# Optimization experiments

Hardware: AMD Instinct MI355X
Metric: run time of the kernel (lower is better)

The kernel has to match this reference:

```python
import jax, jax.numpy as jnp
import numpy as np

N = 100000   # nodes
E = 1600000  # edges (avg degree 16)
F = 64       # input feature dim
H = 64       # hidden dim
O = 64       # conv output dim
C = 2        # channels (x.shape[1])
S = 1000     # number of subgraphs
M = 64       # nodes per subgraph
MH = 128     # MLP hidden
OUT = 1      # MLP output


def setup_inputs() -> dict:
    key = jax.random.key(0)
    ks = jax.random.split(key, 16)
    x = jax.random.normal(ks[0], (N, C, F), jnp.float32)
    edge_index = jax.random.randint(ks[1], (2, E), 0, N, dtype=jnp.int32)
    edge_weight = jax.random.uniform(ks[2], (E,), jnp.float32)
    subG_node = jax.random.randint(ks[3], (S, M), 0, N, dtype=jnp.int32)
    s1 = 1.0 / np.sqrt(F)
    s2 = 1.0 / np.sqrt(H)
    sm1 = 1.0 / np.sqrt(O)
    sm2 = 1.0 / np.sqrt(MH)
    return {
        "x": x,
        "edge_index": edge_index,
        "edge_weight": edge_weight,
        "subG_node": subG_node,
        "W1": jax.random.normal(ks[4], (F, H), jnp.float32) * s1,
        "b1": jnp.zeros((H,), jnp.float32),
        "gn_w": jnp.ones((H,), jnp.float32),
        "gn_b": jnp.zeros((H,), jnp.float32),
        "gn_ms": jnp.ones((H,), jnp.float32),
        "W2": jax.random.normal(ks[5], (H, O), jnp.float32) * s2,
        "b2": jnp.zeros((O,), jnp.float32),
        "mW1": jax.random.normal(ks[6], (O, MH), jnp.float32) * sm1,
        "mb1": jnp.zeros((MH,), jnp.float32),
        "mW2": jax.random.normal(ks[7], (MH, OUT), jnp.float32) * sm2,
        "mb2": jnp.zeros((OUT,), jnp.float32),
    }


def _graph_norm(h, w, b, ms, eps=1e-5):
    # PyG GraphNorm over all nodes (single graph): per-feature stats
    mean = jnp.mean(h, axis=0, keepdims=True)
    out = h - ms * mean
    var = jnp.mean(out * out, axis=0, keepdims=True)
    return w * out * jax.lax.rsqrt(var + eps) + b


def _gcn_layer(h, src, dst, norm, self_norm, W, b, n):
    # GCNConv: h' = D^-1/2 (A + I) D^-1/2 (h @ W) + b
    hw = h @ W                                   # [N, out]
    msg = norm[:, None] * hw[src]                # [E, out] gather
    agg = jax.ops.segment_sum(msg, dst, num_segments=n)  # scatter-add
    agg = agg + self_norm[:, None] * hw          # self-loop term
    return agg + b


def reference(x, edge_index, edge_weight, subG_node,
              W1, b1, gn_w, gn_b, gn_ms, W2, b2, mW1, mb1, mW2, mb2):
    n = x.shape[0]
    src, dst = edge_index[0], edge_index[1]
    # symmetric GCN normalization with self-loops of weight 1
    deg = jax.ops.segment_sum(edge_weight, dst, num_segments=n) + 1.0
    dinv = jax.lax.rsqrt(deg)
    norm = dinv[src] * edge_weight * dinv[dst]   # [E]
    self_norm = dinv * dinv                      # [N]

    def conv_channel(xc):  # xc: [N, F]
        h = _gcn_layer(xc, src, dst, norm, self_norm, W1, b1, n)
        h = _graph_norm(h, gn_w, gn_b, gn_ms)
        h = jax.nn.relu(h)
        return _gcn_layer(h, src, dst, norm, self_norm, W2, b2, n)

    emb = jax.vmap(conv_channel, in_axes=1, out_axes=1)(x)  # [N, C, O]
    emb = jnp.mean(emb, axis=1)                              # [N, O]
    # subgraph pooling: sp @ emb == sum of member-node embeddings
    pooled = jnp.sum(emb[subG_node], axis=1)                 # [S, O]
    h = jax.nn.relu(pooled @ mW1 + mb1)
    return h @ mW2 + mb2                                     # [S, 1]
```

## Files before the change

### kernel.cpp

```cpp
#include <hip/hip_runtime.h>
#include <hip/hip_fp16.h>

#define NNODES 100000
#define NEDGES 1600000
#define NSUB   1000
#define MSUB   64
#define MHID   128

#define WSHIFT 9
#define WIN    512
#define NWIN   ((NNODES + 511) >> 9)
#define NBLK   256
#define CHUNK  (NEDGES / NBLK)

typedef _Float16 f16x8 __attribute__((ext_vector_type(8)));
typedef float    f32x4 __attribute__((ext_vector_type(4)));


__global__ __launch_bounds__(256) void k_hist(const int* __restrict__ dst,
                                              int* __restrict__ block_counts,
                                              int* __restrict__ cursor) {
    __shared__ int hist[NWIN];
    int t = threadIdx.x, b = blockIdx.x;
    if (b == 0 && t == 0) *cursor = 0;
    for (int i = t; i < NWIN; i += 256) hist[i] = 0;
    __syncthreads();
    int e0 = b * CHUNK;
    for (int e = e0 + t; e < e0 + CHUNK; e += 256)
        atomicAdd(&hist[dst[e] >> WSHIFT], 1);
    __syncthreads();
    for (int i = t; i < NWIN; i += 256) block_counts[b * NWIN + i] = hist[i];
}

__global__ __launch_bounds__(256) void k_off(const int* __restrict__ block_counts,
                                             int* __restrict__ cursor,
                                             int* __restrict__ win_base,
                                             int* __restrict__ win_lim,
                                             int* __restrict__ block_off,
                                             float* __restrict__ stats,
                                             unsigned* __restrict__ edges) {
    __shared__ int arr[256];
    __shared__ int red[256];
    __shared__ int base_s;
    int t = threadIdx.x, w = blockIdx.x;
    int own = block_counts[t * NWIN + w];
    arr[t] = own; red[t] = own;
    __syncthreads();
    for (int off = 128; off > 0; off >>= 1) {
        if (t < off) red[t] += red[t + off];
        __syncthreads();
    }
    if (t == 0) base_s = atomicAdd(cursor, red[0]);
    for (int off = 1; off < 256; off <<= 1) {
        int v = (t >= off) ? arr[t - off] : 0;
        __syncthreads();
        arr[t] += v;
        __syncthreads();
    }
    int base = base_s;
    block_off[t * NWIN + w] = base + arr[t] - own;
    if (t == 0) { win_base[w] = base; win_lim[w] = base + red[0]; }
    if (w == 0) {
        stats[t] = 0.0f; stats[t + 256] = 0.0f;
        if (t < 16) edges[NEDGES + t] = 0u;
    }
}

__global__ __launch_bounds__(256) void k_scatter(const int* __restrict__ src,
                                                 const int* __restrict__ dst,
                                                 const float* __restrict__ ew,
                                                 const int* __restrict__ block_off,
                                                 int2* __restrict__ esw) {
    __shared__ int myoff[NWIN];
    int t = threadIdx.x, b = blockIdx.x;
    for (int i = t; i < NWIN; i += 256) myoff[i] = block_off[b * NWIN + i];
    __syncthreads();
    int e0 = b * CHUNK;
    for (int e = e0 + t; e < e0 + CHUNK; e += 256) {
        int d = dst[e];
        int w = d >> WSHIFT;
        int pos = atomicAdd(&myoff[w], 1);
        int dl = d - (w << WSHIFT);
        esw[pos] = make_int2((dl << 17) | src[e], __float_as_int(ew[e]));
    }
}

__global__ __launch_bounds__(256) void k_fill2(const int* __restrict__ win_base,
                                               const int* __restrict__ win_lim,
                                               const int2* __restrict__ esw,
                                               unsigned* __restrict__ edges,
                                               int* __restrict__ row_ptr,
                                               int* __restrict__ cnt,
                                               float* __restrict__ dinv) {
    __shared__ int   cnt_l[WIN];
    __shared__ int   sc[WIN];
    __shared__ int   fill_l[WIN];
    __shared__ float degw[WIN];
    int t = threadIdx.x, w = blockIdx.x;
    #pragma unroll
    for (int i = t; i < WIN; i += 256) { cnt_l[i] = 0; fill_l[i] = 0; degw[i] = 0.f; }
    __syncthreads();
    int e0 = win_base[w], e1 = win_lim[w];
    for (int e = e0 + t; e < e1; e += 256) {
        int2 v = esw[e];
        int dl = ((unsigned)v.x) >> 17;
        atomicAdd(&cnt_l[dl], 1);
        atomicAdd(&degw[dl], __int_as_float(v.y));
    }
    __syncthreads();
    sc[t] = cnt_l[t]; sc[t + 256] = cnt_l[t + 256];
    __syncthreads();
    for (int off = 1; off < WIN; off <<= 1) {
        int v0 = (t >= off) ? sc[t - off] : 0;
        int v1 = (t + 256 >= off) ? sc[t + 256 - off] : 0;
        __syncthreads();
        sc[t] += v0; sc[t + 256] += v1;
        __syncthreads();
    }
    sc[t]       = e0 + sc[t]       - cnt_l[t];
    sc[t + 256] = e0 + sc[t + 256] - cnt_l[t + 256];
    __syncthreads();
    for (int e = e0 + t; e < e1; e += 256) {
        int2 v = esw[e];
        int dl = ((unsigned)v.x) >> 17;
        int pos = sc[dl] + atomicAdd(&fill_l[dl], 1);
        int wq = __float2int_rn(__int_as_float(v.y) * 32767.0f);
        edges[pos] = ((unsigned)wq << 17) | ((unsigned)v.x & 0x1FFFFu);
    }
    __syncthreads();
    #pragma unroll
    for (int i = t; i < WIN; i += 256) {
        int node = (w << WSHIFT) + i;
        if (node < NNODES) {
            row_ptr[node] = sc[i];
            cnt[node]     = cnt_l[i];
            dinv[node]    = rsqrtf(degw[i] + 1.0f);
        }
    }
}


template <bool TR>
__global__ __launch_bounds__(256) void k_gemm(const void* __restrict__ Xv,
                                              const float* __restrict__ Wg,
                                              const float* __restrict__ dinv,
                                              _Float16* __restrict__ Y,
                                              const float* __restrict__ stats,
                                              const float* __restrict__ gn_w,
                                              const float* __restrict__ gn_b,
                                              const float* __restrict__ gn_ms) {
    __shared__ __align__(16) _Float16 ob[4][16 * 72];
    int t = threadIdx.x;
    int wave = t >> 6, lane = t & 63;
    int m = lane & 15, q = lane >> 4;

    f16x8 bf[2][4];
    #pragma unroll
    for (int kb = 0; kb < 2; kb++)
        #pragma unroll
        for (int nt = 0; nt < 4; nt++)
            #pragma unroll
            for (int j = 0; j < 8; j++)
                bf[kb][nt][j] = (_Float16)Wg[(kb * 32 + q * 8 + j) * 64 + nt * 16 + m];

    float ca[16], cb[16];
    if constexpr (TR) {
        int c = m & 1;
        const float inv_n = 1.0f / (float)NNODES;
        #pragma unroll
        for (int kb = 0; kb < 2; kb++)
            #pragma unroll
            for (int j = 0; j < 8; j++) {
                int k = kb * 32 + q * 8 + j;
                int col = c * 64 + k;
                float mean = stats[col] * inv_n;
                float eh2  = stats[128 + col] * inv_n;
                float ms   = gn_ms[k];
                float mm   = ms * mean;
                float var  = eh2 - 2.0f * mm * mean + mm * mm;
                float A = gn_w[k] * rsqrtf(var + 1e-5f);
                ca[kb * 8 + j] = A;
                cb[kb * 8 + j] = gn_b[k] - A * mm;
            }
    }

    int tile = blockIdx.x * 4 + wave;
    int row0 = tile * 16;

    f16x8 af[2];
    if constexpr (!TR) {
        const float* xp = (const float*)Xv + (size_t)(row0 + m) * 64;
        #pragma unroll
        for (int kb = 0; kb < 2; kb++) {
            float4 u0 = *(const float4*)(xp + kb * 32 + q * 8);
            float4 u1 = *(const float4*)(xp + kb * 32 + q * 8 + 4);
            af[kb][0] = (_Float16)u0.x; af[kb][1] = (_Float16)u0.y;
            af[kb][2] = (_Float16)u0.z; af[kb][3] = (_Float16)u0.w;
            af[kb][4] = (_Float16)u1.x; af[kb][5] = (_Float16)u1.y;
            af[kb][6] = (_Float16)u1.z; af[kb][7] = (_Float16)u1.w;
        }
    } else {
        const _Float16* xp = (const _Float16*)Xv + (size_t)(row0 + m) * 64;
        #pragma unroll
        for (int kb = 0; kb < 2; kb++) {
            f16x8 v = *(const f16x8*)(xp + kb * 32 + q * 8);
            #pragma unroll
            for (int j = 0; j < 8; j++) {
                float f = (float)v[j];
                f = fmaxf(ca[kb * 8 + j] * f + cb[kb * 8 + j], 0.0f);
                af[kb][j] = (_Float16)f;
            }
        }
    }

    f32x4 acc[4];
    #pragma unroll
    for (int nt = 0; nt < 4; nt++) {
        acc[nt] = (f32x4){0.f, 0.f, 0.f, 0.f};
        acc[nt] = __builtin_amdgcn_mfma_f32_16x16x32_f16(af[0], bf[0][nt], acc[nt], 0, 0, 0);
        acc[nt] = __builtin_amdgcn_mfma_f32_16x16x32_f16(af[1], bf[1][nt], acc[nt], 0, 0, 0);
    }

    float dv[4];
    #pragma unroll
    for (int i = 0; i < 4; i++) dv[i] = dinv[(row0 + q * 4 + i) >> 1];

    _Float16* obw = ob[wave];
    #pragma unroll
    for (int nt = 0; nt < 4; nt++)
        #pragma unroll
        for (int i = 0; i < 4; i++)
            obw[(q * 4 + i) * 72 + nt * 16 + m] = (_Float16)(acc[nt][i] * dv[i]);
    __syncthreads();

    _Float16* yp = Y + (size_t)row0 * 64;
    #pragma unroll
    for (int s = 0; s < 2; s++) {
        int c8 = s * 64 + lane;
        int r = c8 >> 3, cg = c8 & 7;
        uint4 v = *(const uint4*)(obw + r * 72 + cg * 8);
        *(uint4*)(yp + (size_t)r * 64 + cg * 8) = v;
    }
}


__global__ __launch_bounds__(256) void k_prop(const __half* __restrict__ hw,
                                              const float* __restrict__ bias,
                                              const float* __restrict__ dinv,
                                              const int* __restrict__ row_ptr,
                                              const int* __restrict__ cnt,
                                              const unsigned* __restrict__ edges,
                                              __half* __restrict__ agg) {
    int t = threadIdx.x;
    int lane = t & 63;
    int n = __builtin_amdgcn_readfirstlane(blockIdx.x * 4 + (t >> 6));
    if (n >= NNODES) return;

    int f = lane * 2;
    int feat = f & 63;
    const float qs = 1.0f / 32767.0f;

    float2 bv = *(const float2*)(bias + feat);
    float dv = dinv[n];
    float2 self = __half22float2(*(const __half2*)(hw + (size_t)n * 128 + f));
    float acc0 = self.x;
    float acc1 = self.y;

    int start = row_ptr[n];
    int cn    = cnt[n];
    const unsigned* pp = edges + start;

    int full = cn & ~15;
    int p = 0;
    for (; p < full; p += 16) {
        unsigned e[16];
        #pragma unroll
        for (int i = 0; i < 16; i++) e[i] = pp[p + i];
        float2 h[16];
        #pragma unroll
        for (int i = 0; i < 16; i++) {
            int s = (int)(e[i] & 0x1FFFFu);
            h[i] = __half22float2(*(const __half2*)(hw + (size_t)s * 128 + f));
        }
        #pragma unroll
        for (int i = 0; i < 16; i++) {
            float w = (float)(e[i] >> 17) * qs;
            acc0 += w * h[i].x;
            acc1 += w * h[i].y;
        }
    }
    if (p < cn) {
        unsigned e[16];
        #pragma unroll
        for (int i = 0; i < 16; i++) e[i] = pp[p + i];
        float2 h[16];
        #pragma unroll
        for (int i = 0; i < 16; i++) {
            int s = (int)(e[i] & 0x1FFFFu);
            h[i] = __half22float2(*(const __half2*)(hw + (size_t)s * 128 + f));
        }
        #pragma unroll
        for (int i = 0; i < 16; i++) {
            float w = ((p + i) < cn) ? (float)(e[i] >> 17) * qs : 0.0f;
            acc0 += w * h[i].x;
            acc1 += w * h[i].y;
        }
    }

    *(__half2*)(agg + (size_t)n * 128 + f) =
        __floats2half2_rn(dv * acc0 + bv.x, dv * acc1 + bv.y);
}


__global__ __launch_bounds__(256) void k_stats(const __half* __restrict__ agg,
                                               float* __restrict__ stats) {
    __shared__ float ls[16][128];
    __shared__ float lq[16][128];
    int t = threadIdx.x;
    int cb = (t & 15) * 8;
    int rg = t >> 4;
    float s[8], q[8];
    #pragma unroll
    for (int i = 0; i < 8; i++) { s[i] = 0.f; q[i] = 0.f; }
    for (int r = blockIdx.x * 16 + rg; r < NNODES; r += gridDim.x * 16) {
        uint4 u = *(const uint4*)(agg + (size_t)r * 128 + cb);
        const __half2* h2 = (const __half2*)&u;
        #pragma unroll
        for (int i = 0; i < 4; i++) {
            float2 v = __half22float2(h2[i]);
            s[2*i]   += v.x; q[2*i]   += v.x * v.x;
            s[2*i+1] += v.y; q[2*i+1] += v.y * v.y;
        }
    }
    #pragma unroll
    for (int i = 0; i < 8; i++) { ls[rg][cb + i] = s[i]; lq[rg][cb + i] = q[i]; }
    __syncthreads();
    if (t < 128) {
        float a = 0.f, b = 0.f;
        #pragma unroll
        for (int g = 0; g < 16; g++) { a += ls[g][t]; b += lq[g][t]; }
        atomicAdd(&stats[t], a);
        atomicAdd(&stats[128 + t], b);
    }
}


__global__ __launch_bounds__(256) void k_head(const __half* __restrict__ agg,
                                              const int* __restrict__ subg,
                                              const float* __restrict__ mW1,
                                              const float* __restrict__ mb1,
                                              const float* __restrict__ mW2,
                                              const float* __restrict__ mb2,
                                              float* __restrict__ out) {
    __shared__ int   idx[64];
    __shared__ float pl[4][64];
    __shared__ float red[128];
    int s = blockIdx.x, t = threadIdx.x;
    if (t < 64) idx[t] = subg[s * 64 + t];
    __syncthreads();
    int j = t & 63, grp = t >> 6;
    float acc = 0.f;
    #pragma unroll
    for (int m = grp * 16; m < grp * 16 + 16; m++) {
        int n = idx[m];
        acc += __half2float(agg[(size_t)n * 128 + j]) +
               __half2float(agg[(size_t)n * 128 + 64 + j]);
    }
    pl[grp][j] = acc * 0.5f;
    __syncthreads();
    if (t < 64) pl[0][t] = pl[0][t] + pl[1][t] + pl[2][t] + pl[3][t];
    __syncthreads();
    if (t < 128) {
        float h = mb1[t];
        #pragma unroll
        for (int k = 0; k < 64; k++) h += pl[0][k] * mW1[k * 128 + t];
        h = fmaxf(h, 0.0f);
        red[t] = h * mW2[t];
    }
    __syncthreads();
    for (int off = 64; off > 0; off >>= 1) {
        if (t < off) red[t] += red[t + off];
        __syncthreads();
    }
    if (t == 0) out[s] = red[0] + mb2[0];
}


extern "C" void kernel_launch(void* const* d_in, const int* in_sizes, int n_in,
                              void* d_out, int out_size, void* d_ws, size_t ws_size,
                              hipStream_t stream) {
    const float* x     = (const float*)d_in[0];
    const int*   ei    = (const int*)d_in[1];
    const float* ew    = (const float*)d_in[2];
    const int*   subg  = (const int*)d_in[3];
    const float* W1    = (const float*)d_in[4];
    const float* b1    = (const float*)d_in[5];
    const float* gn_w  = (const float*)d_in[6];
    const float* gn_b  = (const float*)d_in[7];
    const float* gn_ms = (const float*)d_in[8];
    const float* W2    = (const float*)d_in[9];
    const float* b2    = (const float*)d_in[10];
    const float* mW1   = (const float*)d_in[11];
    const float* mb1   = (const float*)d_in[12];
    const float* mW2   = (const float*)d_in[13];
    const float* mb2   = (const float*)d_in[14];
    float* out = (float*)d_out;

    char* w = (char*)d_ws;
    size_t off = 0;
    auto alloc = [&](size_t bytes) {
        void* p = w + off;
        off = (off + bytes + 255) & ~(size_t)255;
        return p;
    };
    float*    dinv    = (float*)   alloc((size_t)NNODES * 4);
    int*      cnt     = (int*)     alloc((size_t)NNODES * 4);
    int*      row_ptr = (int*)     alloc((size_t)NNODES * 4);
    unsigned* edges   = (unsigned*)alloc(((size_t)NEDGES + 16) * 4);
    int2*     esw     = (int2*)    alloc((size_t)NEDGES * 8);
    __half*   hw      = (__half*)  alloc((size_t)NNODES * 128 * 2);
    __half*   agg     = (__half*)  alloc((size_t)NNODES * 128 * 2);
    float*    stats   = (float*)   alloc(512 * 4);
    int*      block_counts = (int*)alloc((size_t)NBLK * NWIN * 4);
    int*      block_off    = (int*)alloc((size_t)NBLK * NWIN * 4);
    int*      win_base     = (int*)alloc(NWIN * 4);
    int*      win_lim      = (int*)alloc(NWIN * 4);
    int*      cursor       = (int*)alloc(256);

    const int* src = ei;
    const int* dst = ei + NEDGES;

    k_hist   <<<NBLK, 256, 0, stream>>>(dst, block_counts, cursor);
    k_off    <<<NWIN, 256, 0, stream>>>(block_counts, cursor, win_base, win_lim,
                                        block_off, stats, edges);
    k_scatter<<<NBLK, 256, 0, stream>>>(src, dst, ew, block_off, esw);
    k_fill2  <<<NWIN, 256, 0, stream>>>(win_base, win_lim, esw, edges, row_ptr, cnt, dinv);

    k_gemm<false><<<3125, 256, 0, stream>>>(x, W1, dinv, (_Float16*)hw,
                                            nullptr, nullptr, nullptr, nullptr);
    k_prop<<<25000, 256, 0, stream>>>(hw, b1, dinv, row_ptr, cnt, edges, agg);

    k_stats<<<512, 256, 0, stream>>>(agg, stats);

    k_gemm<true><<<3125, 256, 0, stream>>>(agg, W2, dinv, (_Float16*)hw,
                                           stats, gn_w, gn_b, gn_ms);
    k_prop<<<25000, 256, 0, stream>>>(hw, b2, dinv, row_ptr, cnt, edges, agg);

    k_head<<<NSUB, 256, 0, stream>>>(agg, subg, mW1, mb1, mW2, mb2, out);
}
```

Measured before the change: 354.6 us.

## Merge phases into cooperative megakernels and skip unused nodes in final propagation

```diff
diff --git a/kernel.cpp b/kernel.cpp
--- a/kernel.cpp
+++ b/kernel.cpp
@@ -1,11 +1,12 @@
 #include <hip/hip_runtime.h>
 #include <hip/hip_fp16.h>
+#include <hip/hip_cooperative_groups.h>
+
+namespace cg = cooperative_groups;
 
 #define NNODES 100000
 #define NEDGES 1600000
 #define NSUB   1000
-#define MSUB   64
-#define MHID   128
 
 #define WSHIFT 9
 #define WIN    512
@@ -16,126 +17,241 @@
 typedef _Float16 f16x8 __attribute__((ext_vector_type(8)));
 typedef float    f32x4 __attribute__((ext_vector_type(4)));
 
-
-__global__ __launch_bounds__(256) void k_hist(const int* __restrict__ dst,
-                                              int* __restrict__ block_counts,
-                                              int* __restrict__ cursor) {
-    __shared__ int hist[NWIN];
+struct Args {
+    const float* x; const int* src; const int* dst; const float* ew; const int* subg;
+    const float* b1; const float* gn_w; const float* gn_b; const float* gn_ms;
+    const float* b2; const float* mW1; const float* mb1; const float* mW2; const float* mb2;
+    float* out;
+    float* dinv; int* cnt; int* row_ptr; int* flags; unsigned* edges; int2* esw;
+    __half* hw; __half* agg; float* stats;
+    int* block_counts; int* block_off; int* win_base; int* win_lim; int* cursor;
+};
+
+union __align__(16) AShm {
+    int hist[NWIN];
+    struct { int arr[256]; int red[256]; int base; } off;
+    int myoff[NWIN];
+    struct { int cnt_l[WIN]; int sc[WIN]; int fill_l[WIN]; float degw[WIN]; } fill;
+};
+struct BShm { float ls[16][128]; float lq[16][128]; };
+struct CShm { int idx[64]; float pl[4][64]; float red[128]; };
+
+
+__device__ __forceinline__ void phase_hist(const Args& a, AShm& sh) {
     int t = threadIdx.x, b = blockIdx.x;
-    if (b == 0 && t == 0) *cursor = 0;
-    for (int i = t; i < NWIN; i += 256) hist[i] = 0;
+    if (b >= NBLK) return;
+    if (b == 0 && t == 0) *a.cursor = 0;
+    if (t < 250) a.flags[a.subg[b * 250 + t]] = 1;
+    for (int i = t; i < NWIN; i += 256) sh.hist[i] = 0;
     __syncthreads();
     int e0 = b * CHUNK;
     for (int e = e0 + t; e < e0 + CHUNK; e += 256)
-        atomicAdd(&hist[dst[e] >> WSHIFT], 1);
-    __syncthreads();
-    for (int i = t; i < NWIN; i += 256) block_counts[b * NWIN + i] = hist[i];
-}
-
-__global__ __launch_bounds__(256) void k_off(const int* __restrict__ block_counts,
-                                             int* __restrict__ cursor,
-                                             int* __restrict__ win_base,
-                                             int* __restrict__ win_lim,
-                                             int* __restrict__ block_off,
-                                             float* __restrict__ stats,
-                                             unsigned* __restrict__ edges) {
-    __shared__ int arr[256];
-    __shared__ int red[256];
-    __shared__ int base_s;
+        atomicAdd(&sh.hist[a.dst[e] >> WSHIFT], 1);
+    __syncthreads();
+    for (int i = t; i < NWIN; i += 256) a.block_counts[b * NWIN + i] = sh.hist[i];
+    if (b == 0) {
+        a.stats[t] = 0.0f; a.stats[t + 256] = 0.0f;
+        if (t < 16) a.edges[NEDGES + t] = 0u;
+    }
+}
+
+__device__ __forceinline__ void phase_off(const Args& a, AShm& sh) {
     int t = threadIdx.x, w = blockIdx.x;
-    int own = block_counts[t * NWIN + w];
-    arr[t] = own; red[t] = own;
+    if (w >= NWIN) return;
+    int own = a.block_counts[t * NWIN + w];
+    sh.off.arr[t] = own; sh.off.red[t] = own;
     __syncthreads();
     for (int off = 128; off > 0; off >>= 1) {
-        if (t < off) red[t] += red[t + off];
-        __syncthreads();
-    }
-    if (t == 0) base_s = atomicAdd(cursor, red[0]);
+        if (t < off) sh.off.red[t] += sh.off.red[t + off];
+        __syncthreads();
+    }
+    if (t == 0) sh.off.base = atomicAdd(a.cursor, sh.off.red[0]);
     for (int off = 1; off < 256; off <<= 1) {
-        int v = (t >= off) ? arr[t - off] : 0;
-        __syncthreads();
-        arr[t] += v;
-        __syncthreads();
-    }
-    int base = base_s;
-    block_off[t * NWIN + w] = base + arr[t] - own;
-    if (t == 0) { win_base[w] = base; win_lim[w] = base + red[0]; }
-    if (w == 0) {
-        stats[t] = 0.0f; stats[t + 256] = 0.0f;
-        if (t < 16) edges[NEDGES + t] = 0u;
-    }
-}
-
-__global__ __launch_bounds__(256) void k_scatter(const int* __restrict__ src,
-                                                 const int* __restrict__ dst,
-                                                 const float* __restrict__ ew,
-                                                 const int* __restrict__ block_off,
-                                                 int2* __restrict__ esw) {
-    __shared__ int myoff[NWIN];
+        int v = (t >= off) ? sh.off.arr[t - off] : 0;
+        __syncthreads();
+        sh.off.arr[t] += v;
+        __syncthreads();
+    }
+    int base = sh.off.base;
+    a.block_off[t * NWIN + w] = base + sh.off.arr[t] - own;
+    if (t == 0) { a.win_base[w] = base; a.win_lim[w] = base + sh.off.red[0]; }
+}
+
+__device__ __forceinline__ void phase_scatter(const Args& a, AShm& sh) {
     int t = threadIdx.x, b = blockIdx.x;
-    for (int i = t; i < NWIN; i += 256) myoff[i] = block_off[b * NWIN + i];
+    if (b >= NBLK) return;
+    for (int i = t; i < NWIN; i += 256) sh.myoff[i] = a.block_off[b * NWIN + i];
     __syncthreads();
     int e0 = b * CHUNK;
     for (int e = e0 + t; e < e0 + CHUNK; e += 256) {
-        int d = dst[e];
+        int d = a.dst[e];
         int w = d >> WSHIFT;
-        int pos = atomicAdd(&myoff[w], 1);
+        int pos = atomicAdd(&sh.myoff[w], 1);
         int dl = d - (w << WSHIFT);
-        esw[pos] = make_int2((dl << 17) | src[e], __float_as_int(ew[e]));
-    }
-}
-
-__global__ __launch_bounds__(256) void k_fill2(const int* __restrict__ win_base,
-                                               const int* __restrict__ win_lim,
-                                               const int2* __restrict__ esw,
-                                               unsigned* __restrict__ edges,
-                                               int* __restrict__ row_ptr,
-                                               int* __restrict__ cnt,
-                                               float* __restrict__ dinv) {
-    __shared__ int   cnt_l[WIN];
-    __shared__ int   sc[WIN];
-    __shared__ int   fill_l[WIN];
-    __shared__ float degw[WIN];
+        a.esw[pos] = make_int2((dl << 17) | a.src[e], __float_as_int(a.ew[e]));
+    }
+}
+
+__device__ __forceinline__ void phase_fill2(const Args& a, AShm& sh) {
     int t = threadIdx.x, w = blockIdx.x;
-    #pragma unroll
-    for (int i = t; i < WIN; i += 256) { cnt_l[i] = 0; fill_l[i] = 0; degw[i] = 0.f; }
-    __syncthreads();
-    int e0 = win_base[w], e1 = win_lim[w];
+    if (w >= NWIN) return;
+    #pragma unroll
+    for (int i = t; i < WIN; i += 256) { sh.fill.cnt_l[i] = 0; sh.fill.fill_l[i] = 0; sh.fill.degw[i] = 0.f; }
+    __syncthreads();
+    int e0 = a.win_base[w], e1 = a.win_lim[w];
     for (int e = e0 + t; e < e1; e += 256) {
-        int2 v = esw[e];
+        int2 v = a.esw[e];
         int dl = ((unsigned)v.x) >> 17;
-        atomicAdd(&cnt_l[dl], 1);
-        atomicAdd(&degw[dl], __int_as_float(v.y));
-    }
-    __syncthreads();
-    sc[t] = cnt_l[t]; sc[t + 256] = cnt_l[t + 256];
+        atomicAdd(&sh.fill.cnt_l[dl], 1);
+        atomicAdd(&sh.fill.degw[dl], __int_as_float(v.y));
+    }
+    __syncthreads();
+    sh.fill.sc[t] = sh.fill.cnt_l[t]; sh.fill.sc[t + 256] = sh.fill.cnt_l[t + 256];
     __syncthreads();
     for (int off = 1; off < WIN; off <<= 1) {
-        int v0 = (t >= off) ? sc[t - off] : 0;
-        int v1 = (t + 256 >= off) ? sc[t + 256 - off] : 0;
-        __syncthreads();
-        sc[t] += v0; sc[t + 256] += v1;
-        __syncthreads();
-    }
-    sc[t]       = e0 + sc[t]       - cnt_l[t];
-    sc[t + 256] = e0 + sc[t + 256] - cnt_l[t + 256];
+        int v0 = (t >= off) ? sh.fill.sc[t - off] : 0;
+        int v1 = (t + 256 >= off) ? sh.fill.sc[t + 256 - off] : 0;
+        __syncthreads();
+        sh.fill.sc[t] += v0; sh.fill.sc[t + 256] += v1;
+        __syncthreads();
+    }
+    sh.fill.sc[t]       = e0 + sh.fill.sc[t]       - sh.fill.cnt_l[t];
+    sh.fill.sc[t + 256] = e0 + sh.fill.sc[t + 256] - sh.fill.cnt_l[t + 256];
     __syncthreads();
     for (int e = e0 + t; e < e1; e += 256) {
-        int2 v = esw[e];
+        int2 v = a.esw[e];
         int dl = ((unsigned)v.x) >> 17;
-        int pos = sc[dl] + atomicAdd(&fill_l[dl], 1);
+        int pos = sh.fill.sc[dl] + atomicAdd(&sh.fill.fill_l[dl], 1);
         int wq = __float2int_rn(__int_as_float(v.y) * 32767.0f);
-        edges[pos] = ((unsigned)wq << 17) | ((unsigned)v.x & 0x1FFFFu);
+        a.edges[pos] = ((unsigned)wq << 17) | ((unsigned)v.x & 0x1FFFFu);
     }
     __syncthreads();
     #pragma unroll
     for (int i = t; i < WIN; i += 256) {
         int node = (w << WSHIFT) + i;
         if (node < NNODES) {
-            row_ptr[node] = sc[i];
-            cnt[node]     = cnt_l[i];
-            dinv[node]    = rsqrtf(degw[i] + 1.0f);
-        }
+            a.row_ptr[node] = sh.fill.sc[i];
+            a.cnt[node]     = sh.fill.cnt_l[i];
+            a.dinv[node]    = rsqrtf(sh.fill.degw[i] + 1.0f);
+        }
+    }
+}
+
+template <bool USE_FLAGS>
+__device__ __forceinline__ void phase_prop(const Args& a, const float* bias) {
+    int t = threadIdx.x;
+    int lane = t & 63, wv = t >> 6;
+    int f = lane * 2, feat = f & 63;
+    const float qs = 1.0f / 32767.0f;
+    float2 bv = *(const float2*)(bias + feat);
+    for (int g = blockIdx.x; g < 25000; g += (int)gridDim.x) {
+        int n = __builtin_amdgcn_readfirstlane(g * 4 + wv);
+        if (USE_FLAGS && a.flags[n] != 1) continue;
+        float dv = a.dinv[n];
+        float2 self = __half22float2(*(const __half2*)(a.hw + (size_t)n * 128 + f));
+        float acc0 = self.x, acc1 = self.y;
+        int start = a.row_ptr[n];
+        int cn    = a.cnt[n];
+        const unsigned* pp = a.edges + start;
+        int full = cn & ~15, p = 0;
+        for (; p < full; p += 16) {
+            unsigned e[16];
+            #pragma unroll
+            for (int i = 0; i < 16; i++) e[i] = pp[p + i];
+            float2 h[16];
+            #pragma unroll
+            for (int i = 0; i < 16; i++) {
+                int s = (int)(e[i] & 0x1FFFFu);
+                h[i] = __half22float2(*(const __half2*)(a.hw + (size_t)s * 128 + f));
+            }
+            #pragma unroll
+            for (int i = 0; i < 16; i++) {
+                float w = (float)(e[i] >> 17) * qs;
+                acc0 += w * h[i].x;
+                acc1 += w * h[i].y;
+            }
+        }
+        if (p < cn) {
+            unsigned e[16];
+            #pragma unroll
+            for (int i = 0; i < 16; i++) e[i] = pp[p + i];
+            float2 h[16];
+            #pragma unroll
+            for (int i = 0; i < 16; i++) {
+                int s = (int)(e[i] & 0x1FFFFu);
+                h[i] = __half22float2(*(const __half2*)(a.hw + (size_t)s * 128 + f));
+            }
+            #pragma unroll
+            for (int i = 0; i < 16; i++) {
+                float w = ((p + i) < cn) ? (float)(e[i] >> 17) * qs : 0.0f;
+                acc0 += w * h[i].x;
+                acc1 += w * h[i].y;
+            }
+        }
+        *(__half2*)(a.agg + (size_t)n * 128 + f) =
+            __floats2half2_rn(dv * acc0 + bv.x, dv * acc1 + bv.y);
+    }
+}
+
+__device__ __forceinline__ void phase_stats(const Args& a, BShm& sh) {
+    int t = threadIdx.x;
+    int cb = (t & 15) * 8, rg = t >> 4;
+    float s[8], q[8];
+    #pragma unroll
+    for (int i = 0; i < 8; i++) { s[i] = 0.f; q[i] = 0.f; }
+    for (int r = blockIdx.x * 16 + rg; r < NNODES; r += (int)gridDim.x * 16) {
+        uint4 u = *(const uint4*)(a.agg + (size_t)r * 128 + cb);
+        const __half2* h2 = (const __half2*)&u;
+        #pragma unroll
+        for (int i = 0; i < 4; i++) {
+            float2 v = __half22float2(h2[i]);
+            s[2*i]   += v.x; q[2*i]   += v.x * v.x;
+            s[2*i+1] += v.y; q[2*i+1] += v.y * v.y;
+        }
+    }
+    #pragma unroll
+    for (int i = 0; i < 8; i++) { sh.ls[rg][cb + i] = s[i]; sh.lq[rg][cb + i] = q[i]; }
+    __syncthreads();
+    if (t < 128) {
+        float aa = 0.f, b = 0.f;
+        #pragma unroll
+        for (int g = 0; g < 16; g++) { aa += sh.ls[g][t]; b += sh.lq[g][t]; }
+        atomicAdd(&a.stats[t], aa);
+        atomicAdd(&a.stats[128 + t], b);
+    }
+}
+
+__device__ __forceinline__ void phase_head(const Args& a, CShm& sh) {
+    int t = threadIdx.x;
+    int j = t & 63, grp = t >> 6;
+    for (int s = blockIdx.x; s < NSUB; s += (int)gridDim.x) {
+        if (t < 64) sh.idx[t] = a.subg[s * 64 + t];
+        __syncthreads();
+        float acc = 0.f;
+        #pragma unroll
+        for (int m = grp * 16; m < grp * 16 + 16; m++) {
+            int n = sh.idx[m];
+            acc += __half2float(a.agg[(size_t)n * 128 + j]) +
+                   __half2float(a.agg[(size_t)n * 128 + 64 + j]);
+        }
+        sh.pl[grp][j] = acc * 0.5f;
+        __syncthreads();
+        if (t < 64) sh.pl[0][t] = sh.pl[0][t] + sh.pl[1][t] + sh.pl[2][t] + sh.pl[3][t];
+        __syncthreads();
+        if (t < 128) {
+            float h = a.mb1[t];
+            #pragma unroll
+            for (int k = 0; k < 64; k++) h += sh.pl[0][k] * a.mW1[k * 128 + t];
+            h = fmaxf(h, 0.0f);
+            sh.red[t] = h * a.mW2[t];
+        }
+        __syncthreads();
+        for (int off = 64; off > 0; off >>= 1) {
+            if (t < off) sh.red[t] += sh.red[t + off];
+            __syncthreads();
+        }
+        if (t == 0) a.out[s] = sh.red[0] + a.mb2[0];
+        __syncthreads();
     }
 }
 
@@ -237,174 +353,73 @@
     #pragma unroll
     for (int s = 0; s < 2; s++) {
         int c8 = s * 64 + lane;
-        int r = c8 >> 3, cg = c8 & 7;
-        uint4 v = *(const uint4*)(obw + r * 72 + cg * 8);
-        *(uint4*)(yp + (size_t)r * 64 + cg * 8) = v;
-    }
-}
-
-
-__global__ __launch_bounds__(256) void k_prop(const __half* __restrict__ hw,
-                                              const float* __restrict__ bias,
-                                              const float* __restrict__ dinv,
-                                              const int* __restrict__ row_ptr,
-                                              const int* __restrict__ cnt,
-                                              const unsigned* __restrict__ edges,
-                                              __half* __restrict__ agg) {
-    int t = threadIdx.x;
-    int lane = t & 63;
-    int n = __builtin_amdgcn_readfirstlane(blockIdx.x * 4 + (t >> 6));
-    if (n >= NNODES) return;
-
-    int f = lane * 2;
-    int feat = f & 63;
-    const float qs = 1.0f / 32767.0f;
-
-    float2 bv = *(const float2*)(bias + feat);
-    float dv = dinv[n];
-    float2 self = __half22float2(*(const __half2*)(hw + (size_t)n * 128 + f));
-    float acc0 = self.x;
-    float acc1 = self.y;
-
-    int start = row_ptr[n];
-    int cn    = cnt[n];
-    const unsigned* pp = edges + start;
-
-    int full = cn & ~15;
-    int p = 0;
-    for (; p < full; p += 16) {
-        unsigned e[16];
-        #pragma unroll
-        for (int i = 0; i < 16; i++) e[i] = pp[p + i];
-        float2 h[16];
-        #pragma unroll
-        for (int i = 0; i < 16; i++) {
-            int s = (int)(e[i] & 0x1FFFFu);
-            h[i] = __half22float2(*(const __half2*)(hw + (size_t)s * 128 + f));
-        }
-        #pragma unroll
-        for (int i = 0; i < 16; i++) {
-            float w = (float)(e[i] >> 17) * qs;
-            acc0 += w * h[i].x;
-            acc1 += w * h[i].y;
-        }
-    }
-    if (p < cn) {
-        unsigned e[16];
-        #pragma unroll
-        for (int i = 0; i < 16; i++) e[i] = pp[p + i];
-        float2 h[16];
-        #pragma unroll
-        for (int i = 0; i < 16; i++) {
-            int s = (int)(e[i] & 0x1FFFFu);
-            h[i] = __half22float2(*(const __half2*)(hw + (size_t)s * 128 + f));
-        }
-        #pragma unroll
-        for (int i = 0; i < 16; i++) {
-            float w = ((p + i) < cn) ? (float)(e[i] >> 17) * qs : 0.0f;
-            acc0 += w * h[i].x;
-            acc1 += w * h[i].y;
-        }
-    }
-
-    *(__half2*)(agg + (size_t)n * 128 + f) =
-        __floats2half2_rn(dv * acc0 + bv.x, dv * acc1 + bv.y);
-}
-
-
-__global__ __launch_bounds__(256) void k_stats(const __half* __restrict__ agg,
-                                               float* __restrict__ stats) {
-    __shared__ float ls[16][128];
-    __shared__ float lq[16][128];
-    int t = threadIdx.x;
-    int cb = (t & 15) * 8;
-    int rg = t >> 4;
-    float s[8], q[8];
-    #pragma unroll
-    for (int i = 0; i < 8; i++) { s[i] = 0.f; q[i] = 0.f; }
-    for (int r = blockIdx.x * 16 + rg; r < NNODES; r += gridDim.x * 16) {
-        uint4 u = *(const uint4*)(agg + (size_t)r * 128 + cb);
-        const __half2* h2 = (const __half2*)&u;
-        #pragma unroll
-        for (int i = 0; i < 4; i++) {
-            float2 v = __half22float2(h2[i]);
-            s[2*i]   += v.x; q[2*i]   += v.x * v.x;
-            s[2*i+1] += v.y; q[2*i+1] += v.y * v.y;
-        }
-    }
-    #pragma unroll
-    for (int i = 0; i < 8; i++) { ls[rg][cb + i] = s[i]; lq[rg][cb + i] = q[i]; }
-    __syncthreads();
-    if (t < 128) {
-        float a = 0.f, b = 0.f;
-        #pragma unroll
-        for (int g = 0; g < 16; g++) { a += ls[g][t]; b += lq[g][t]; }
-        atomicAdd(&stats[t], a);
-        atomicAdd(&stats[128 + t], b);
-    }
-}
-
-
-__global__ __launch_bounds__(256) void k_head(const __half* __restrict__ agg,
-                                              const int* __restrict__ subg,
-                                              const float* __restrict__ mW1,
-                                              const float* __restrict__ mb1,
-                                              const float* __restrict__ mW2,
-                                              const float* __restrict__ mb2,
-                                              float* __restrict__ out) {
-    __shared__ int   idx[64];
-    __shared__ float pl[4][64];
-    __shared__ float red[128];
-    int s = blockIdx.x, t = threadIdx.x;
-    if (t < 64) idx[t] = subg[s * 64 + t];
-    __syncthreads();
-    int j = t & 63, grp = t >> 6;
-    float acc = 0.f;
-    #pragma unroll
-    for (int m = grp * 16; m < grp * 16 + 16; m++) {
-        int n = idx[m];
-        acc += __half2float(agg[(size_t)n * 128 + j]) +
-               __half2float(agg[(size_t)n * 128 + 64 + j]);
-    }
-    pl[grp][j] = acc * 0.5f;
-    __syncthreads();
-    if (t < 64) pl[0][t] = pl[0][t] + pl[1][t] + pl[2][t] + pl[3][t];
-    __syncthreads();
-    if (t < 128) {
-        float h = mb1[t];
-        #pragma unroll
-        for (int k = 0; k < 64; k++) h += pl[0][k] * mW1[k * 128 + t];
-        h = fmaxf(h, 0.0f);
-        red[t] = h * mW2[t];
-    }
-    __syncthreads();
-    for (int off = 64; off > 0; off >>= 1) {
-        if (t < off) red[t] += red[t + off];
-        __syncthreads();
-    }
-    if (t == 0) out[s] = red[0] + mb2[0];
-}
+        int r = c8 >> 3, cg2 = c8 & 7;
+        uint4 v = *(const uint4*)(obw + r * 72 + cg2 * 8);
+        *(uint4*)(yp + (size_t)r * 64 + cg2 * 8) = v;
+    }
+}
+
+
+__global__ void megaA(Args a) {
+    __shared__ AShm sh;
+    cg::grid_group g = cg::this_grid();
+    phase_hist(a, sh);
+    g.sync();
+    phase_off(a, sh);
+    g.sync();
+    phase_scatter(a, sh);
+    g.sync();
+    phase_fill2(a, sh);
+}
+
+__global__ __launch_bounds__(256, 6) void megaB(Args a) {
+    __shared__ BShm sh;
+    cg::grid_group g = cg::this_grid();
+    phase_prop<false>(a, a.b1);
+    g.sync();
+    phase_stats(a, sh);
+}
+
+__global__ __launch_bounds__(256, 6) void megaC(Args a) {
+    __shared__ CShm sh;
+    cg::grid_group g = cg::this_grid();
+    phase_prop<true>(a, a.b2);
+    g.sync();
+    phase_head(a, sh);
+}
+
+__global__ void w_hist(Args a)    { __shared__ AShm sh; phase_hist(a, sh); }
+__global__ void w_off(Args a)     { __shared__ AShm sh; phase_off(a, sh); }
+__global__ void w_scatter(Args a) { __shared__ AShm sh; phase_scatter(a, sh); }
+__global__ void w_fill2(Args a)   { __shared__ AShm sh; phase_fill2(a, sh); }
+__global__ __launch_bounds__(256) void w_prop1(Args a) { phase_prop<false>(a, a.b1); }
+__global__ __launch_bounds__(256) void w_stats(Args a) { __shared__ BShm sh; phase_stats(a, sh); }
+__global__ __launch_bounds__(256) void w_prop2(Args a) { phase_prop<true>(a, a.b2); }
+__global__ __launch_bounds__(256) void w_head(Args a)  { __shared__ CShm sh; phase_head(a, sh); }
 
 
 extern "C" void kernel_launch(void* const* d_in, const int* in_sizes, int n_in,
                               void* d_out, int out_size, void* d_ws, size_t ws_size,
                               hipStream_t stream) {
-    const float* x     = (const float*)d_in[0];
-    const int*   ei    = (const int*)d_in[1];
-    const float* ew    = (const float*)d_in[2];
-    const int*   subg  = (const int*)d_in[3];
-    const float* W1    = (const float*)d_in[4];
-    const float* b1    = (const float*)d_in[5];
-    const float* gn_w  = (const float*)d_in[6];
-    const float* gn_b  = (const float*)d_in[7];
-    const float* gn_ms = (const float*)d_in[8];
-    const float* W2    = (const float*)d_in[9];
-    const float* b2    = (const float*)d_in[10];
-    const float* mW1   = (const float*)d_in[11];
-    const float* mb1   = (const float*)d_in[12];
-    const float* mW2   = (const float*)d_in[13];
-    const float* mb2   = (const float*)d_in[14];
-    float* out = (float*)d_out;
+    Args a;
+    a.x     = (const float*)d_in[0];
+    const int* ei = (const int*)d_in[1];
+    a.src   = ei;
+    a.dst   = ei + NEDGES;
+    a.ew    = (const float*)d_in[2];
+    a.subg  = (const int*)d_in[3];
+    const float* W1 = (const float*)d_in[4];
+    a.b1    = (const float*)d_in[5];
+    a.gn_w  = (const float*)d_in[6];
+    a.gn_b  = (const float*)d_in[7];
+    a.gn_ms = (const float*)d_in[8];
+    const float* W2 = (const float*)d_in[9];
+    a.b2    = (const float*)d_in[10];
+    a.mW1   = (const float*)d_in[11];
+    a.mb1   = (const float*)d_in[12];
+    a.mW2   = (const float*)d_in[13];
+    a.mb2   = (const float*)d_in[14];
+    a.out   = (float*)d_out;
 
     char* w = (char*)d_ws;
     size_t off = 0;
@@ -413,38 +428,55 @@
         off = (off + bytes + 255) & ~(size_t)255;
         return p;
     };
-    float*    dinv    = (float*)   alloc((size_t)NNODES * 4);
-    int*      cnt     = (int*)     alloc((size_t)NNODES * 4);
-    int*      row_ptr = (int*)     alloc((size_t)NNODES * 4);
-    unsigned* edges   = (unsigned*)alloc(((size_t)NEDGES + 16) * 4);
-    int2*     esw     = (int2*)    alloc((size_t)NEDGES * 8);
-    __half*   hw      = (__half*)  alloc((size_t)NNODES * 128 * 2);
-    __half*   agg     = (__half*)  alloc((size_t)NNODES * 128 * 2);
-    float*    stats   = (float*)   alloc(512 * 4);
-    int*      block_counts = (int*)alloc((size_t)NBLK * NWIN * 4);
-    int*      block_off    = (int*)alloc((size_t)NBLK * NWIN * 4);
-    int*      win_base     = (int*)alloc(NWIN * 4);
-    int*      win_lim      = (int*)alloc(NWIN * 4);
-    int*      cursor       = (int*)alloc(256);
-
-    const int* src = ei;
-    const int* dst = ei + NEDGES;
-
-    k_hist   <<<NBLK, 256, 0, stream>>>(dst, block_counts, cursor);
-    k_off    <<<NWIN, 256, 0, stream>>>(block_counts, cursor, win_base, win_lim,
-                                        block_off, stats, edges);
-    k_scatter<<<NBLK, 256, 0, stream>>>(src, dst, ew, block_off, esw);
-    k_fill2  <<<NWIN, 256, 0, stream>>>(win_base, win_lim, esw, edges, row_ptr, cnt, dinv);
-
-    k_gemm<false><<<3125, 256, 0, stream>>>(x, W1, dinv, (_Float16*)hw,
+    a.dinv    = (float*)   alloc((size_t)NNODES * 4);
+    a.cnt     = (int*)     alloc((size_t)NNODES * 4);
+    a.row_ptr = (int*)     alloc((size_t)NNODES * 4);
+    a.flags   = (int*)     alloc((size_t)NNODES * 4);
+    a.edges   = (unsigned*)alloc(((size_t)NEDGES + 16) * 4);
+    a.esw     = (int2*)    alloc((size_t)NEDGES * 8);
+    a.hw      = (__half*)  alloc((size_t)NNODES * 128 * 2);
+    a.agg     = (__half*)  alloc((size_t)NNODES * 128 * 2);
+    a.stats   = (float*)   alloc(512 * 4);
+    a.block_counts = (int*)alloc((size_t)NBLK * NWIN * 4);
+    a.block_off    = (int*)alloc((size_t)NBLK * NWIN * 4);
+    a.win_base     = (int*)alloc(NWIN * 4);
+    a.win_lim      = (int*)alloc(NWIN * 4);
+    a.cursor       = (int*)alloc(256);
+
+    int perCU = 0;
+    bool coop = (hipOccupancyMaxActiveBlocksPerMultiprocessor(&perCU, (const void*)megaB, 256, 0)
+                 == hipSuccess) && perCU >= 1;
+    if (perCU > 6) perCU = 6;
+    int NB = (coop ? perCU : 6) * 256;
+
+    void* pa[] = { (void*)&a };
+
+    bool okA = coop &&
+        hipLaunchCooperativeKernel((const void*)megaA, dim3(NBLK), dim3(256), pa, 0, stream) == hipSuccess;
+    if (!okA) {
+        w_hist   <<<NBLK, 256, 0, stream>>>(a);
+        w_off    <<<NWIN, 256, 0, stream>>>(a);
+        w_scatter<<<NBLK, 256, 0, stream>>>(a);
+        w_fill2  <<<NWIN, 256, 0, stream>>>(a);
+    }
+
+    k_gemm<false><<<3125, 256, 0, stream>>>(a.x, W1, a.dinv, (_Float16*)a.hw,
                                             nullptr, nullptr, nullptr, nullptr);
-    k_prop<<<25000, 256, 0, stream>>>(hw, b1, dinv, row_ptr, cnt, edges, agg);
-
-    k_stats<<<512, 256, 0, stream>>>(agg, stats);
-
-    k_gemm<true><<<3125, 256, 0, stream>>>(agg, W2, dinv, (_Float16*)hw,
-                                           stats, gn_w, gn_b, gn_ms);
-    k_prop<<<25000, 256, 0, stream>>>(hw, b2, dinv, row_ptr, cnt, edges, agg);
-
-    k_head<<<NSUB, 256, 0, stream>>>(agg, subg, mW1, mb1, mW2, mb2, out);
-}
+
+    bool okB = coop &&
+        hipLaunchCooperativeKernel((const void*)megaB, dim3(NB), dim3(256), pa, 0, stream) == hipSuccess;
+    if (!okB) {
+        w_prop1<<<25000, 256, 0, stream>>>(a);
+        w_stats<<<512, 256, 0, stream>>>(a);
+    }
+
+    k_gemm<true><<<3125, 256, 0, stream>>>(a.agg, W2, a.dinv, (_Float16*)a.hw,
+                                           a.stats, a.gn_w, a.gn_b, a.gn_ms);
+
+    bool okC = coop &&
+        hipLaunchCooperativeKernel((const void*)megaC, dim3(NB), dim3(256), pa, 0, stream) == hipSuccess;
+    if (!okC) {
+        w_prop2<<<25000, 256, 0, stream>>>(a);
+        w_head <<<NSUB, 256, 0, stream>>>(a);
+    }
+}
```

Result: slower. 828.9 us (+133.8%).
